# Kernel optimization log

Hardware: AMD Instinct MI355X
Metric: run time of the kernel (lower is better)

The kernel has to match this reference:

```python
import jax, jax.numpy as jnp
import numpy as np

B, I, H = 512, 2048, 2048


def setup_inputs() -> dict:
    key = jax.random.key(0)
    ks = jax.random.split(key, 14)
    s = 0.02  # weight init scale
    inp = {
        "inputs": jax.random.normal(ks[0], (B, I), jnp.float32),
        "states": jax.random.normal(ks[1], (2, B, H), jnp.float32),
        "Wi": jax.random.normal(ks[2], (I, H), jnp.float32) * s,
        "Ui": jax.random.normal(ks[3], (H, H), jnp.float32) * s,
        "bi": jnp.zeros((H,), jnp.float32),
        "Wf": jax.random.normal(ks[4], (I, H), jnp.float32) * s,
        "Uf": jax.random.normal(ks[5], (H, H), jnp.float32) * s,
        "bf": jnp.zeros((H,), jnp.float32),
        "Wg": jax.random.normal(ks[6], (I, H), jnp.float32) * s,
        "Ug": jax.random.normal(ks[7], (H, H), jnp.float32) * s,
        "bg": jnp.zeros((H,), jnp.float32),
        "Wc": jax.random.normal(ks[8], (I, H), jnp.float32) * s,
        "Uc": jax.random.normal(ks[9], (H, H), jnp.float32) * s,
        "bc": jnp.zeros((H,), jnp.float32),
    }
    return inp


def reference(inputs, states, Wi, Ui, bi, Wf, Uf, bf, Wg, Ug, bg, Wc, Uc, bc):
    # Faithful to the original cell, including its quirks:
    # recurrent matmuls use states[0] (prevstate); c mixes states[1] (prevoutput).
    prevstate, prevoutput = states[0], states[1]  # [B,H] each
    i = jax.nn.sigmoid(inputs @ Wi + prevstate @ Ui + bi)
    f = jax.nn.sigmoid(inputs @ Wf + prevstate @ Uf + bf)
    g = jax.nn.sigmoid(inputs @ Wg + prevstate @ Ug + bg)
    c_ = jnp.tanh(inputs @ Wc + prevstate @ Uc + bc)
    c = f * prevoutput + i * c_
    state = g * jnp.tanh(c)
    return c, jnp.stack([state, c])
```

## Files before the change

kernel.cpp:

```cpp
#include <hip/hip_runtime.h>

#define BH (512*2048)
#define BHA 1048576ull
#define PPLANE (512ull*8192ull)
#define PLANE_BYTES (PPLANE*2ull)
#define AB_ELEMS (2ull*512*2048)

typedef __attribute__((ext_vector_type(8))) short short8;
typedef __attribute__((ext_vector_type(4))) float floatx4;
typedef __attribute__((ext_vector_type(4))) unsigned int uint4v;
typedef __attribute__((ext_vector_type(8))) unsigned short ushort8v;

#define GLOAD_LDS16(g, l) __builtin_amdgcn_global_load_lds( \
    (const __attribute__((address_space(1))) unsigned int*)(g), \
    (__attribute__((address_space(3))) unsigned int*)(l), 16, 0, 0)

__device__ inline unsigned pk2(float a, float b){
    unsigned ua = __builtin_bit_cast(unsigned, a) + 0x8000u;
    unsigned ub = __builtin_bit_cast(unsigned, b) + 0x8000u;
    return __builtin_amdgcn_perm(ub, ua, 0x07060302u);
}
__device__ inline unsigned short f2bf1(float x){
    return (unsigned short)((__builtin_bit_cast(unsigned, x) + 0x8000u) >> 16);
}
__device__ inline float bf2f(unsigned short s){
    return __builtin_bit_cast(float, ((unsigned)s) << 16);
}
__device__ inline int swz(int r, int g){ return r*4 + (g ^ ((r>>1)&3)); }
__device__ inline float fsig(float x){ return __builtin_amdgcn_rcpf(1.f + __expf(-x)); }
__device__ inline float ftanh(float x){ return 2.f*fsig(2.f*x) - 1.f; }

__global__ __launch_bounds__(256) void prep_act(
    const float* __restrict__ inputs, const float* __restrict__ states,
    unsigned short* __restrict__ Ab)
{
    const size_t off = ((size_t)blockIdx.x * 256 + threadIdx.x) * 8;
    const float* src = (off < BHA) ? (inputs + off) : (states + (off - BHA));
    floatx4 v0 = *(const floatx4*)src;
    floatx4 v1 = *(const floatx4*)(src + 4);
    uint4v w;
    w.x = pk2(v0[0],v0[1]); w.y = pk2(v0[2],v0[3]);
    w.z = pk2(v1[0],v1[1]); w.w = pk2(v1[2],v1[3]);
    *(uint4v*)(Ab + off) = w;
}

__global__ __launch_bounds__(256, 3) void gemm_fused(
    const float* __restrict__ Wi, const float* __restrict__ Ui,
    const float* __restrict__ Wf, const float* __restrict__ Uf,
    const float* __restrict__ Wg, const float* __restrict__ Ug,
    const float* __restrict__ Wc, const float* __restrict__ Uc,
    const unsigned short* __restrict__ Ab, unsigned short* __restrict__ P)
{
    __shared__ unsigned short As[2][4096];
    __shared__ unsigned short Bs[2][4096];

    const int t = threadIdx.x, lane = t & 63, wave = t >> 6;
    const int nblk = blockIdx.x, gate = nblk >> 4, nb = nblk & 15;
    const int m0 = blockIdx.y * 128, z = blockIdx.z;

    const float* Bsel;
    if (z < 2) { switch (gate){ case 0: Bsel=Wi; break; case 1: Bsel=Wf; break;
                                case 2: Bsel=Wg; break; default: Bsel=Wc; } }
    else       { switch (gate){ case 0: Bsel=Ui; break; case 1: Bsel=Uf; break;
                                case 2: Bsel=Ug; break; default: Bsel=Uc; } }
    const int n   = t & 127;
    const int o0  = t >> 7;
    const int swk = (n >> 1) & 3;
    const float* Bp0 = Bsel + ((size_t)((z & 1) * 1024 + o0 * 8)) * 2048
                            + nb * 128 + n;
    const float* Bp1 = Bp0 + (size_t)16 * 2048;

    const unsigned short* Abase = Ab + (size_t)(z >> 1) * BHA
                                     + (size_t)m0 * 2048 + (z & 1) * 1024;
    const int i0 = wave * 2, i1 = wave * 2 + 1;
    const int arow = lane >> 2;
    const int agr  = (lane & 3) ^ ((lane >> 3) & 3);
    const unsigned short* ag0 = Abase + (size_t)(i0*16 + arow) * 2048 + agr * 8;
    const unsigned short* ag1 = Abase + (size_t)(i1*16 + arow) * 2048 + agr * 8;

    floatx4 acc[4][4];
    #pragma unroll
    for (int i = 0; i < 4; i++)
        #pragma unroll
        for (int j = 0; j < 4; j++)
            acc[i][j] = (floatx4){0.f,0.f,0.f,0.f};

    const int wm = (wave & 1) * 64, wn = (wave >> 1) * 64;
    const int row16 = lane & 15, g4 = lane >> 4;
    const int fgx = ((g4 ^ ((row16 >> 1) & 3)) << 3);

    const int wb0 = n * 32 + (((o0    ) ^ swk) << 3);
    const int wb1 = n * 32 + (((o0 + 2) ^ swk) << 3);

    float u0[8], u1[8];

    GLOAD_LDS16(ag0, &As[0][i0 * 512]);
    GLOAD_LDS16(ag1, &As[0][i1 * 512]);
    #pragma unroll
    for (int j = 0; j < 8; j++) u0[j] = Bp0[(size_t)j * 2048];
    #pragma unroll
    for (int j = 0; j < 8; j++) u1[j] = Bp1[(size_t)j * 2048];
    *(uint4v*)&Bs[0][wb0] = (uint4v){pk2(u0[0],u0[1]), pk2(u0[2],u0[3]),
                                     pk2(u0[4],u0[5]), pk2(u0[6],u0[7])};
    *(uint4v*)&Bs[0][wb1] = (uint4v){pk2(u1[0],u1[1]), pk2(u1[2],u1[3]),
                                     pk2(u1[4],u1[5]), pk2(u1[6],u1[7])};
    __syncthreads();

    for (int kk = 0; kk < 32; kk++) {
        const int cur = kk & 1;
        if (kk < 31) {
            const int nxt = cur ^ 1;
            GLOAD_LDS16(ag0 + (kk+1)*32, &As[nxt][i0 * 512]);
            GLOAD_LDS16(ag1 + (kk+1)*32, &As[nxt][i1 * 512]);
            const float* q0 = Bp0 + (size_t)(kk+1) * 65536;
            const float* q1 = Bp1 + (size_t)(kk+1) * 65536;
            #pragma unroll
            for (int j = 0; j < 8; j++) u0[j] = q0[(size_t)j * 2048];
            #pragma unroll
            for (int j = 0; j < 8; j++) u1[j] = q1[(size_t)j * 2048];
        }
        short8 afr[4], bfr[4];
        #pragma unroll
        for (int mi = 0; mi < 4; mi++)
            afr[mi] = *(const short8*)&As[cur][(wm + mi*16 + row16)*32 + fgx];
        #pragma unroll
        for (int ni = 0; ni < 4; ni++)
            bfr[ni] = *(const short8*)&Bs[cur][(wn + ni*16 + row16)*32 + fgx];
        #pragma unroll
        for (int mi = 0; mi < 4; mi++)
            #pragma unroll
            for (int ni = 0; ni < 4; ni++)
                acc[mi][ni] = __builtin_amdgcn_mfma_f32_16x16x32_bf16(
                    afr[mi], bfr[ni], acc[mi][ni], 0, 0, 0);
        if (kk < 31) {
            const int nxt = cur ^ 1;
            *(uint4v*)&Bs[nxt][wb0] = (uint4v){pk2(u0[0],u0[1]), pk2(u0[2],u0[3]),
                                               pk2(u0[4],u0[5]), pk2(u0[6],u0[7])};
            *(uint4v*)&Bs[nxt][wb1] = (uint4v){pk2(u1[0],u1[1]), pk2(u1[2],u1[3]),
                                               pk2(u1[4],u1[5]), pk2(u1[6],u1[7])};
        }
        __syncthreads();
    }

    unsigned short* dst = P + (size_t)z * PPLANE;
    const int gbase = gate * 2048 + nb * 128;
    #pragma unroll
    for (int mi = 0; mi < 4; mi++)
        #pragma unroll
        for (int ni = 0; ni < 4; ni++)
            #pragma unroll
            for (int j = 0; j < 4; j++) {
                int row = m0 + wm + mi*16 + g4*4 + j;
                int col = gbase + wn + ni*16 + row16;
                dst[(size_t)row * 8192 + col] = f2bf1(acc[mi][ni][j]);
            }
}

__global__ __launch_bounds__(256, 2) void gemm_tile(
    const float* __restrict__ inputs, const float* __restrict__ states,
    const float* __restrict__ Wi, const float* __restrict__ Ui,
    const float* __restrict__ Wf, const float* __restrict__ Uf,
    const float* __restrict__ Wg, const float* __restrict__ Ug,
    const float* __restrict__ Wc, const float* __restrict__ Uc,
    unsigned short* __restrict__ P, int KB)
{
    __shared__ uint4v As[2][512];
    __shared__ uint4v Bs[2][512];

    const int t = threadIdx.x;
    const int m0 = blockIdx.y * 128;
    const int z = blockIdx.z;
    const int nblk = blockIdx.x;
    const int gate = nblk >> 4;
    const int c0 = (nblk & 15) * 128;
    const int gk = z * KB;

    const float* Abase; const float* Bsel; int ko;
    if (gk < 2048) {
        Abase = inputs; ko = gk;
        switch (gate){ case 0: Bsel=Wi; break; case 1: Bsel=Wf; break;
                       case 2: Bsel=Wg; break; default: Bsel=Wc; }
    } else {
        Abase = states; ko = gk - 2048;
        switch (gate){ case 0: Bsel=Ui; break; case 1: Bsel=Uf; break;
                       case 2: Bsel=Ug; break; default: Bsel=Uc; }
    }
    const int NIT = KB >> 5;

    const int lane = t & 63, wave = t >> 6;
    const int wm = (wave & 1) * 64, wn = (wave >> 1) * 64;
    const int row16 = lane & 15, g4 = lane >> 4;
    const int ar = t >> 2, ag = t & 3;
    const int bn = t & 127, bg2 = (t >> 7) * 2;

    const float* Ap = Abase + (size_t)(m0 + ar) * 2048 + ko + ag * 8;
    const float* Bp = Bsel + (size_t)ko * 2048 + c0 + bn;

    floatx4 acc[4][4];
    #pragma unroll
    for (int i = 0; i < 4; i++)
        #pragma unroll
        for (int j = 0; j < 4; j++)
            acc[i][j] = (floatx4){0.f,0.f,0.f,0.f};

    floatx4 a0,a1,a2,a3; float b0[8], b1[8];
    a0 = *(const floatx4*)Ap;             a1 = *(const floatx4*)(Ap + 4);
    a2 = *(const floatx4*)(Ap + 64*2048); a3 = *(const floatx4*)(Ap + 64*2048 + 4);
    #pragma unroll
    for (int j = 0; j < 8; j++) b0[j] = Bp[(size_t)(bg2*8 + j) * 2048];
    #pragma unroll
    for (int j = 0; j < 8; j++) b1[j] = Bp[(size_t)(bg2*8 + 8 + j) * 2048];
    {
        uint4v w;
        w.x=pk2(a0[0],a0[1]); w.y=pk2(a0[2],a0[3]); w.z=pk2(a1[0],a1[1]); w.w=pk2(a1[2],a1[3]);
        As[0][swz(ar, ag)] = w;
        w.x=pk2(a2[0],a2[1]); w.y=pk2(a2[2],a2[3]); w.z=pk2(a3[0],a3[1]); w.w=pk2(a3[2],a3[3]);
        As[0][swz(ar+64, ag)] = w;
        w.x=pk2(b0[0],b0[1]); w.y=pk2(b0[2],b0[3]); w.z=pk2(b0[4],b0[5]); w.w=pk2(b0[6],b0[7]);
        Bs[0][swz(bn, bg2)] = w;
        w.x=pk2(b1[0],b1[1]); w.y=pk2(b1[2],b1[3]); w.z=pk2(b1[4],b1[5]); w.w=pk2(b1[6],b1[7]);
        Bs[0][swz(bn, bg2+1)] = w;
    }

    for (int kk = 0; kk < NIT; kk++) {
        __syncthreads();
        const int cur = kk & 1;
        if (kk + 1 < NIT) {
            const float* ap = Ap + (kk+1) * 32;
            a0 = *(const floatx4*)ap;             a1 = *(const floatx4*)(ap + 4);
            a2 = *(const floatx4*)(ap + 64*2048); a3 = *(const floatx4*)(ap + 64*2048 + 4);
            const float* bp = Bp + (size_t)(kk+1) * 32 * 2048;
            #pragma unroll
            for (int j = 0; j < 8; j++) b0[j] = bp[(size_t)(bg2*8 + j) * 2048];
            #pragma unroll
            for (int j = 0; j < 8; j++) b1[j] = bp[(size_t)(bg2*8 + 8 + j) * 2048];
        }
        short8 afr[4], bfr[4];
        #pragma unroll
        for (int mi = 0; mi < 4; mi++)
            afr[mi] = *(const short8*)&As[cur][swz(wm + mi*16 + row16, g4)];
        #pragma unroll
        for (int ni = 0; ni < 4; ni++)
            bfr[ni] = *(const short8*)&Bs[cur][swz(wn + ni*16 + row16, g4)];
        #pragma unroll
        for (int mi = 0; mi < 4; mi++)
            #pragma unroll
            for (int ni = 0; ni < 4; ni++)
                acc[mi][ni] = __builtin_amdgcn_mfma_f32_16x16x32_bf16(
                    afr[mi], bfr[ni], acc[mi][ni], 0, 0, 0);
        if (kk + 1 < NIT) {
            const int nxt = cur ^ 1;
            uint4v w;
            w.x=pk2(a0[0],a0[1]); w.y=pk2(a0[2],a0[3]); w.z=pk2(a1[0],a1[1]); w.w=pk2(a1[2],a1[3]);
            As[nxt][swz(ar, ag)] = w;
            w.x=pk2(a2[0],a2[1]); w.y=pk2(a2[2],a2[3]); w.z=pk2(a3[0],a3[1]); w.w=pk2(a3[2],a3[3]);
            As[nxt][swz(ar+64, ag)] = w;
            w.x=pk2(b0[0],b0[1]); w.y=pk2(b0[2],b0[3]); w.z=pk2(b0[4],b0[5]); w.w=pk2(b0[6],b0[7]);
            Bs[nxt][swz(bn, bg2)] = w;
            w.x=pk2(b1[0],b1[1]); w.y=pk2(b1[2],b1[3]); w.z=pk2(b1[4],b1[5]); w.w=pk2(b1[6],b1[7]);
            Bs[nxt][swz(bn, bg2+1)] = w;
        }
    }

    unsigned short* dst = P + (size_t)z * PPLANE;
    const int gbase = gate * 2048 + c0;
    #pragma unroll
    for (int mi = 0; mi < 4; mi++)
        #pragma unroll
        for (int ni = 0; ni < 4; ni++)
            #pragma unroll
            for (int j = 0; j < 4; j++) {
                int row = m0 + wm + mi*16 + g4*4 + j;
                int col = gbase + wn + ni*16 + row16;
                dst[(size_t)row * 8192 + col] = f2bf1(acc[mi][ni][j]);
            }
}

__global__ __launch_bounds__(256) void combine_kernel(
    float* __restrict__ out, const unsigned short* __restrict__ P,
    const float* __restrict__ states,
    const float* __restrict__ bi, const float* __restrict__ bfv,
    const float* __restrict__ bg, const float* __restrict__ bc, int nz)
{
    const int idx = (blockIdx.x * 256 + threadIdx.x) * 8;
    const int row = idx >> 11;
    const int h = idx & 2047;
    const size_t base = (size_t)row * 8192 + h;

    float xi[8], xf[8], xg[8], xc[8];
    #pragma unroll
    for (int e = 0; e < 8; e++) {
        xi[e] = bi[h+e]; xf[e] = bfv[h+e]; xg[e] = bg[h+e]; xc[e] = bc[h+e];
    }
    for (int z = 0; z < nz; z++) {
        const unsigned short* Pz = P + (size_t)z * PPLANE;
        ushort8v vi = *(const ushort8v*)&Pz[base];
        ushort8v vf = *(const ushort8v*)&Pz[base + 2048];
        ushort8v vg = *(const ushort8v*)&Pz[base + 4096];
        ushort8v vc = *(const ushort8v*)&Pz[base + 6144];
        #pragma unroll
        for (int e = 0; e < 8; e++) {
            xi[e] += bf2f(vi[e]); xf[e] += bf2f(vf[e]);
            xg[e] += bf2f(vg[e]); xc[e] += bf2f(vc[e]);
        }
    }

    const float* po = states + BH;
    floatx4 pov[2];
    pov[0] = *(const floatx4*)&po[idx];
    pov[1] = *(const floatx4*)&po[idx + 4];

    floatx4 vcv[2], vsv[2];
    #pragma unroll
    for (int q = 0; q < 2; q++)
        #pragma unroll
        for (int j = 0; j < 4; j++) {
            int e = q*4 + j;
            float c = fsig(xf[e]) * pov[q][j] + fsig(xi[e]) * ftanh(xc[e]);
            vcv[q][j] = c;
            vsv[q][j] = fsig(xg[e]) * ftanh(c);
        }
    #pragma unroll
    for (int q = 0; q < 2; q++) {
        *(floatx4*)&out[idx + q*4]        = vcv[q];
        *(floatx4*)&out[BH + idx + q*4]   = vsv[q];
        *(floatx4*)&out[2*BH + idx + q*4] = vcv[q];
    }
}

extern "C" void kernel_launch(void* const* d_in, const int* in_sizes, int n_in,
                              void* d_out, int out_size, void* d_ws, size_t ws_size,
                              hipStream_t stream) {
    const float* inputs = (const float*)d_in[0];
    const float* states = (const float*)d_in[1];
    const float* Wi = (const float*)d_in[2];
    const float* Ui = (const float*)d_in[3];
    const float* bi = (const float*)d_in[4];
    const float* Wf = (const float*)d_in[5];
    const float* Uf = (const float*)d_in[6];
    const float* bf = (const float*)d_in[7];
    const float* Wg = (const float*)d_in[8];
    const float* Ug = (const float*)d_in[9];
    const float* bg = (const float*)d_in[10];
    const float* Wc = (const float*)d_in[11];
    const float* Uc = (const float*)d_in[12];
    const float* bc = (const float*)d_in[13];
    float* out = (float*)d_out;

    const size_t need = (AB_ELEMS + 4 * PPLANE) * 2;
    if (ws_size >= need) {
        unsigned short* Ab = (unsigned short*)d_ws;
        unsigned short* P  = Ab + AB_ELEMS;
        prep_act<<<1024, 256, 0, stream>>>(inputs, states, Ab);
        gemm_fused<<<dim3(64, 4, 4), 256, 0, stream>>>(Wi, Ui, Wf, Uf,
                                                       Wg, Ug, Wc, Uc, Ab, P);
        combine_kernel<<<BH / (8 * 256), 256, 0, stream>>>(out, P, states,
                                                           bi, bf, bg, bc, 4);
    } else {
        unsigned short* P = (unsigned short*)d_ws;
        const int nz = (ws_size >= 4 * PLANE_BYTES) ? 4 : 2;
        const int KB = 4096 / nz;
        dim3 grid(64, 4, nz);
        gemm_tile<<<grid, 256, 0, stream>>>(inputs, states, Wi, Ui, Wf, Uf,
                                            Wg, Ug, Wc, Uc, P, KB);
        combine_kernel<<<BH / (8 * 256), 256, 0, stream>>>(out, P, states,
                                                           bi, bf, bg, bc, nz);
    }
}
```

Before: 246.3 us.

## Deepen B prefetch to two tiles and stage A through registers

The GEMM tile kernel now keeps two K-tiles of fp32 B weights in flight in registers, unrolling the K loop by two with ping-pong register sets. A-operand staging moves from direct global-to-LDS loads to ordinary vector loads into registers followed by swizzled LDS writes. The aim is to hide more global-load latency behind the MFMA work. The cost is higher register pressure, which may lower occupancy, and extra VGPR traffic for A.

```diff
diff --git a/kernel.cpp b/kernel.cpp
--- a/kernel.cpp
+++ b/kernel.cpp
@@ -10,10 +10,6 @@
 typedef __attribute__((ext_vector_type(4))) float floatx4;
 typedef __attribute__((ext_vector_type(4))) unsigned int uint4v;
 typedef __attribute__((ext_vector_type(8))) unsigned short ushort8v;
-
-#define GLOAD_LDS16(g, l) __builtin_amdgcn_global_load_lds( \
-    (const __attribute__((address_space(1))) unsigned int*)(g), \
-    (__attribute__((address_space(3))) unsigned int*)(l), 16, 0, 0)
 
 __device__ inline unsigned pk2(float a, float b){
     unsigned ua = __builtin_bit_cast(unsigned, a) + 0x8000u;
@@ -65,18 +61,20 @@
                                 case 2: Bsel=Ug; break; default: Bsel=Uc; } }
     const int n   = t & 127;
     const int o0  = t >> 7;
-    const int swk = (n >> 1) & 3;
+    const int swkB = (n >> 1) & 3;
     const float* Bp0 = Bsel + ((size_t)((z & 1) * 1024 + o0 * 8)) * 2048
                             + nb * 128 + n;
     const float* Bp1 = Bp0 + (size_t)16 * 2048;
-
-    const unsigned short* Abase = Ab + (size_t)(z >> 1) * BHA
-                                     + (size_t)m0 * 2048 + (z & 1) * 1024;
-    const int i0 = wave * 2, i1 = wave * 2 + 1;
-    const int arow = lane >> 2;
-    const int agr  = (lane & 3) ^ ((lane >> 3) & 3);
-    const unsigned short* ag0 = Abase + (size_t)(i0*16 + arow) * 2048 + agr * 8;
-    const unsigned short* ag1 = Abase + (size_t)(i1*16 + arow) * 2048 + agr * 8;
+    const int wb0 = n * 32 + (((o0    ) ^ swkB) << 3);
+    const int wb1 = n * 32 + (((o0 + 2) ^ swkB) << 3);
+
+    const int ar = t >> 1, ah = t & 1;
+    const int swkA = (ar >> 1) & 3;
+    const unsigned short* Aptr = Ab + (size_t)(z >> 1) * BHA
+                               + (size_t)(m0 + ar) * 2048 + (z & 1) * 1024
+                               + ah * 16;
+    const int wa0 = ar * 32 + (((2*ah    ) ^ swkA) << 3);
+    const int wa1 = ar * 32 + (((2*ah + 1) ^ swkA) << 3);
 
     floatx4 acc[4][4];
     #pragma unroll
@@ -89,58 +87,75 @@
     const int row16 = lane & 15, g4 = lane >> 4;
     const int fgx = ((g4 ^ ((row16 >> 1) & 3)) << 3);
 
-    const int wb0 = n * 32 + (((o0    ) ^ swk) << 3);
-    const int wb1 = n * 32 + (((o0 + 2) ^ swk) << 3);
-
-    float u0[8], u1[8];
-
-    GLOAD_LDS16(ag0, &As[0][i0 * 512]);
-    GLOAD_LDS16(ag1, &As[0][i1 * 512]);
-    #pragma unroll
-    for (int j = 0; j < 8; j++) u0[j] = Bp0[(size_t)j * 2048];
-    #pragma unroll
-    for (int j = 0; j < 8; j++) u1[j] = Bp1[(size_t)j * 2048];
-    *(uint4v*)&Bs[0][wb0] = (uint4v){pk2(u0[0],u0[1]), pk2(u0[2],u0[3]),
-                                     pk2(u0[4],u0[5]), pk2(u0[6],u0[7])};
-    *(uint4v*)&Bs[0][wb1] = (uint4v){pk2(u1[0],u1[1]), pk2(u1[2],u1[3]),
-                                     pk2(u1[4],u1[5]), pk2(u1[6],u1[7])};
+    float uB0a[8], uB0b[8], uB1a[8], uB1b[8];
+    uint4v uA0, uA1;
+
+#define B_LOAD(d0, d1, tile) do { \
+    const float* q0_ = Bp0 + (size_t)(tile) * 65536; \
+    const float* q1_ = Bp1 + (size_t)(tile) * 65536; \
+    _Pragma("unroll") for (int j = 0; j < 8; j++) d0[j] = q0_[(size_t)j * 2048]; \
+    _Pragma("unroll") for (int j = 0; j < 8; j++) d1[j] = q1_[(size_t)j * 2048]; \
+} while(0)
+
+#define B_WRITE(buf, s0, s1) do { \
+    *(uint4v*)&Bs[buf][wb0] = (uint4v){pk2(s0[0],s0[1]), pk2(s0[2],s0[3]), \
+                                       pk2(s0[4],s0[5]), pk2(s0[6],s0[7])}; \
+    *(uint4v*)&Bs[buf][wb1] = (uint4v){pk2(s1[0],s1[1]), pk2(s1[2],s1[3]), \
+                                       pk2(s1[4],s1[5]), pk2(s1[6],s1[7])}; \
+} while(0)
+
+#define A_LOAD(tile) do { \
+    const unsigned short* ap_ = Aptr + (size_t)(tile) * 32; \
+    uA0 = *(const uint4v*)ap_; uA1 = *(const uint4v*)(ap_ + 8); \
+} while(0)
+
+#define A_WRITE(buf) do { \
+    *(uint4v*)&As[buf][wa0] = uA0; *(uint4v*)&As[buf][wa1] = uA1; \
+} while(0)
+
+#define FRAGS_MFMA(buf) do { \
+    short8 afr[4], bfr[4]; \
+    _Pragma("unroll") for (int mi = 0; mi < 4; mi++) \
+        afr[mi] = *(const short8*)&As[buf][(wm + mi*16 + row16)*32 + fgx]; \
+    _Pragma("unroll") for (int ni = 0; ni < 4; ni++) \
+        bfr[ni] = *(const short8*)&Bs[buf][(wn + ni*16 + row16)*32 + fgx]; \
+    _Pragma("unroll") for (int mi = 0; mi < 4; mi++) \
+        _Pragma("unroll") for (int ni = 0; ni < 4; ni++) \
+            acc[mi][ni] = __builtin_amdgcn_mfma_f32_16x16x32_bf16( \
+                afr[mi], bfr[ni], acc[mi][ni], 0, 0, 0); \
+} while(0)
+
+    B_LOAD(uB0a, uB0b, 0);
+    B_LOAD(uB1a, uB1b, 1);
+    A_LOAD(0);
+    A_WRITE(0);
+    B_WRITE(0, uB0a, uB0b);
     __syncthreads();
 
-    for (int kk = 0; kk < 32; kk++) {
-        const int cur = kk & 1;
-        if (kk < 31) {
-            const int nxt = cur ^ 1;
-            GLOAD_LDS16(ag0 + (kk+1)*32, &As[nxt][i0 * 512]);
-            GLOAD_LDS16(ag1 + (kk+1)*32, &As[nxt][i1 * 512]);
-            const float* q0 = Bp0 + (size_t)(kk+1) * 65536;
-            const float* q1 = Bp1 + (size_t)(kk+1) * 65536;
-            #pragma unroll
-            for (int j = 0; j < 8; j++) u0[j] = q0[(size_t)j * 2048];
-            #pragma unroll
-            for (int j = 0; j < 8; j++) u1[j] = q1[(size_t)j * 2048];
-        }
-        short8 afr[4], bfr[4];
-        #pragma unroll
-        for (int mi = 0; mi < 4; mi++)
-            afr[mi] = *(const short8*)&As[cur][(wm + mi*16 + row16)*32 + fgx];
-        #pragma unroll
-        for (int ni = 0; ni < 4; ni++)
-            bfr[ni] = *(const short8*)&Bs[cur][(wn + ni*16 + row16)*32 + fgx];
-        #pragma unroll
-        for (int mi = 0; mi < 4; mi++)
-            #pragma unroll
-            for (int ni = 0; ni < 4; ni++)
-                acc[mi][ni] = __builtin_amdgcn_mfma_f32_16x16x32_bf16(
-                    afr[mi], bfr[ni], acc[mi][ni], 0, 0, 0);
-        if (kk < 31) {
-            const int nxt = cur ^ 1;
-            *(uint4v*)&Bs[nxt][wb0] = (uint4v){pk2(u0[0],u0[1]), pk2(u0[2],u0[3]),
-                                               pk2(u0[4],u0[5]), pk2(u0[6],u0[7])};
-            *(uint4v*)&Bs[nxt][wb1] = (uint4v){pk2(u1[0],u1[1]), pk2(u1[2],u1[3]),
-                                               pk2(u1[4],u1[5]), pk2(u1[6],u1[7])};
-        }
+    for (int kk = 0; kk < 32; kk += 2) {
+        if (kk < 30) { B_LOAD(uB0a, uB0b, kk + 2); }
+        A_LOAD(kk + 1);
+        FRAGS_MFMA(0);
+        A_WRITE(1);
+        B_WRITE(1, uB1a, uB1b);
         __syncthreads();
-    }
+        if (kk < 30) {
+            B_LOAD(uB1a, uB1b, kk + 3);
+            A_LOAD(kk + 2);
+        }
+        FRAGS_MFMA(1);
+        if (kk < 30) {
+            A_WRITE(0);
+            B_WRITE(0, uB0a, uB0b);
+        }
+        __syncthreads();
+    }
+
+#undef B_LOAD
+#undef B_WRITE
+#undef A_LOAD
+#undef A_WRITE
+#undef FRAGS_MFMA
 
     unsigned short* dst = P + (size_t)z * PPLANE;
     const int gbase = gate * 2048 + nb * 128;
```

After: 253.4 us. 2.9% more time.
